# Performance work log

Measured on AMD Instinct MI355X. Metric: run time of the kernel, lower is better.

The kernel has to match this reference:

```python
import jax, jax.numpy as jnp
import numpy as np

NEG_INF = -1e30
EPS = 1e-7  # keras.backend.epsilon()


def _ctc_loss(y_true, y_pred):
    """Faithful CTC loss matching keras ctc_batch_cost + tf v1 ctc_loss.

    y_true: [B, L] int labels (no blanks), all rows full length L.
    y_pred: [B, T, C] probabilities; tf ctc_loss re-softmaxes log(p+eps).
    Blank index = C - 1. Returns loss [B, 1].
    """
    B, T, C = y_pred.shape
    L = y_true.shape[1]
    S = 2 * L + 1
    blank = C - 1

    # keras passes log(y_pred+eps) as logits; tf ctc_loss applies softmax
    lp = jax.nn.log_softmax(jnp.log(y_pred + EPS), axis=-1)  # [B,T,C]

    # extended label sequence: blank, l0, blank, l1, ..., blank  [B,S]
    ext = jnp.full((B, S), blank, dtype=y_true.dtype)
    ext = ext.at[:, 1::2].set(y_true)

    # skip transition (s-2 -> s) allowed iff ext[s] != blank and ext[s] != ext[s-2]
    same_as_2back = jnp.concatenate(
        [jnp.ones((B, 2), bool), ext[:, 2:] == ext[:, :-2]], axis=1)
    can_skip = (ext != blank) & (~same_as_2back)  # [B,S]

    # emission log-prob of each lattice state at each time: [B,T,S]
    lp_ext = jnp.take_along_axis(lp, ext[:, None, :], axis=2)

    # alpha init at t=0: only states 0 (blank) and 1 (first label) reachable
    alpha0 = jnp.full((B, S), NEG_INF, dtype=lp.dtype)
    alpha0 = alpha0.at[:, 0].set(lp_ext[:, 0, 0])
    alpha0 = alpha0.at[:, 1].set(lp_ext[:, 0, 1])

    pad1 = jnp.full((B, 1), NEG_INF, dtype=lp.dtype)
    pad2 = jnp.full((B, 2), NEG_INF, dtype=lp.dtype)

    def step(alpha, lp_t):
        a_stay = alpha
        a_prev = jnp.concatenate([pad1, alpha[:, :-1]], axis=1)
        a_skip = jnp.where(can_skip,
                           jnp.concatenate([pad2, alpha[:, :-2]], axis=1),
                           NEG_INF)
        m = jnp.maximum(a_stay, jnp.maximum(a_prev, a_skip))
        lse = m + jnp.log(jnp.exp(a_stay - m) + jnp.exp(a_prev - m)
                          + jnp.exp(a_skip - m))
        return lse + lp_t, None

    # scan over remaining T-1 time steps
    alphaT, _ = jax.lax.scan(step, alpha0, jnp.swapaxes(lp_ext, 0, 1)[1:])

    # total log-likelihood: end at last blank or last label
    loglik = jnp.logaddexp(alphaT[:, S - 1], alphaT[:, S - 2])
    return -loglik[:, None]  # [B,1], matches expand_dims(..., 1)


def setup_inputs() -> dict:
    key = jax.random.key(0)
    k1, k2 = jax.random.split(key)
    B, T, C, L = 128, 1024, 128, 128
    y_true = jax.random.randint(k1, (B, L), 0, C - 1, dtype=jnp.int32)
    y_pred = jax.random.uniform(k2, (B, T, C), dtype=jnp.float32)
    return {"y_true": y_true, "y_pred": y_pred}


def reference(y_true, y_pred):
    return _ctc_loss(y_true, y_pred)
```

## Files before the change

### kernel.cpp

```cpp
#include <hip/hip_runtime.h>

#define TT 1024
#define CC 128
#define LL 128
#define EPSF 1e-7f
#define LN2F 0.69314718055994531f

#define LOG2F(x) __builtin_amdgcn_logf(x)

typedef unsigned int uint;

template <int CTRL>
__device__ __forceinline__ int dpp_i(int old_, int x) {
  return __builtin_amdgcn_update_dpp(old_, x, CTRL, 0xf, 0xf, false);
}
__device__ __forceinline__ float dpp_shr1_f32(float x) {
  return __uint_as_float((uint)__builtin_amdgcn_update_dpp(
      0, (int)__float_as_uint(x), 0x138, 0xf, 0xf, true));
}

__device__ __forceinline__ uint bf16bits(float x) {
  uint u = __float_as_uint(x);
  return (u + 0x7fffu + ((u >> 16) & 1u)) >> 16;
}

#define GL16(gp, lp)                                            \
  __builtin_amdgcn_global_load_lds(                             \
      (const __attribute__((address_space(1))) void*)(gp),      \
      (__attribute__((address_space(3))) void*)(lp), 16, 0, 0)

__global__ __launch_bounds__(512) void prep_kernel(const int* __restrict__ yt,
                                                   const float* __restrict__ yp,
                                                   uint* __restrict__ ET,
                                                   float* __restrict__ EB) {
  const int tid = threadIdx.x;
  const int w = tid >> 6;
  const int L = tid & 63;
  const int b = blockIdx.x >> 7;
  const int tg = blockIdx.x & 127;
  const int t = tg * 8 + w;

  __shared__ float rowp[8][130];
  __shared__ uint tp[64][9];

  const float* P = yp + ((size_t)b * TT + t) * CC;
  const float2 v = *(const float2*)(P + 2 * L);
  float x = (v.x + EPSF) + (v.y + EPSF);
#pragma unroll
  for (int off = 32; off > 0; off >>= 1) x += __shfl_xor(x, off);
  const float r = 1.0f / x;
  const float er = EPSF * r;
  *(float2*)&rowp[w][2 * L] =
      make_float2(__builtin_fmaf(v.x, r, er), __builtin_fmaf(v.y, r, er));
  const int2 lab = *(const int2*)(yt + b * LL + 2 * L);
  if (L == 63) EB[b * TT + t] = __builtin_fmaf(v.y, r, er);
  __syncthreads();
  const float p1 = rowp[w][lab.x];
  const float p2 = rowp[w][lab.y];
  tp[L][w] = (bf16bits(p2) << 16) | bf16bits(p1);
  __syncthreads();
  if (tid < 128) {
    const int g4 = tid >> 6, Lo = tid & 63;
    uint4 val;
    val.x = tp[Lo][g4 * 4 + 0];
    val.y = tp[Lo][g4 * 4 + 1];
    val.z = tp[Lo][g4 * 4 + 2];
    val.w = tp[Lo][g4 * 4 + 3];
    ((uint4*)ET)[((size_t)(b * 256 + tg * 2 + g4) << 6) + Lo] = val;
  }
}


#define CTC_STEP(wv, pbf)                                   \
  do {                                                      \
    const float p1 = __uint_as_float((wv) << 16);           \
    const float p2 = __uint_as_float((wv) & 0xffff0000u);   \
    const float pb = (pbf);                                 \
    const float p3 = dpp_shr1_f32(a3);                      \
    const float n0 = (a0 + p3) * pb;                        \
    const float n1 = __builtin_fmaf(s1f, p3, a0 + a1) * p1; \
    const float n2 = (a2 + a1) * pb;                        \
    const float n3 = __builtin_fmaf(s3f, a1, a3 + a2) * p2; \
    const float n4 = (a4 + a3) * pb;                        \
    a0 = n0; a1 = n1; a2 = n2; a3 = n3; a4 = n4;            \
  } while (0)

#define CTC_QUAD(et, eb) \
  do {                   \
    CTC_STEP(et.x, eb.x); \
    CTC_STEP(et.y, eb.y); \
    CTC_STEP(et.z, eb.z); \
    CTC_STEP(et.w, eb.w); \
  } while (0)

#define CTC_RESCALE()                                                \
  do {                                                               \
    const float m = fmaxf(fmaxf(fmaxf(a0, a1), fmaxf(a2, a3)), a4);  \
    int ke = (int)(__float_as_uint(m) >> 23);                        \
    ke = max(ke, dpp_i<0x111>(ke, ke));                              \
    ke = max(ke, dpp_i<0x112>(ke, ke));                              \
    ke = max(ke, dpp_i<0x114>(ke, ke));                              \
    ke = max(ke, dpp_i<0x118>(ke, ke));                              \
    ke = max(ke, dpp_i<0x142>(ke, ke));                              \
    ke = max(ke, dpp_i<0x143>(ke, ke));                              \
    ke = __builtin_amdgcn_readlane(ke, 63);                          \
    int e = ke - 227;             \
    e = e < -127 ? -127 : e;                                         \
    const float sc = __uint_as_float((uint)(127 - e) << 23);         \
    a0 *= sc; a1 *= sc; a2 *= sc; a3 *= sc; a4 *= sc;                \
    ell += e;                                                        \
  } while (0)

__global__ __launch_bounds__(64) void scan_kernel(const int* __restrict__ yt,
                                                  const uint* __restrict__ ET,
                                                  const float* __restrict__ EB,
                                                  float* __restrict__ out) {
  const int b = blockIdx.x;
  const int L = threadIdx.x & 63;

  __shared__ uint4 ETl[4][8][64];
  __shared__ float4 EBl[256];

  const int2 lab = *(const int2*)(yt + b * LL + 2 * L);
  const int labm1 = __shfl_up(lab.y, 1);
  const float s1f = ((L > 0) && (lab.x != labm1)) ? 1.0f : 0.0f;
  const float s3f = (lab.y != lab.x) ? 1.0f : 0.0f;

  const uint4* Et = (const uint4*)ET + ((size_t)b << 14) + L;
  const float* Bp = EB + b * TT;

#pragma unroll
  for (int k = 0; k < 4; ++k)
    GL16(Bp + k * 256 + L * 4, (char*)EBl + k * 1024);
#pragma unroll
  for (int g = 0; g < 8; ++g) GL16(Et + g * 64, &ETl[0][g][0]);
#pragma unroll
  for (int g = 0; g < 8; ++g) GL16(Et + (8 + g) * 64, &ETl[1][g][0]);
  asm volatile("s_waitcnt vmcnt(8)" ::: "memory");

  uint4 etA = ETl[0][0][L], etB;
  float4 ebA = EBl[0], ebB;

  float a0 = (L == 0) ? 0x1.0p100f : 0.0f;
  float a1 = 0.0f, a2 = 0.0f, a3 = 0.0f, a4 = 0.0f;
  int ell = -100;

#pragma unroll 1
  for (int i = 0; i < 32; ++i) {
    {
      const int ip = (i + 2 < 32) ? (i + 2) : 31;
      const uint4* src = Et + (size_t)ip * 512;
      uint4* dst = &ETl[(i + 2) & 3][0][0];
#pragma unroll
      for (int g = 0; g < 8; ++g) GL16(src + g * 64, dst + g * 64);
    }
    const uint4* cur = &ETl[i & 3][0][0];
    const int ebi = i * 8;
    etB = cur[1 * 64 + L]; ebB = EBl[ebi + 1];
    CTC_QUAD(etA, ebA);
    etA = cur[2 * 64 + L]; ebA = EBl[ebi + 2];
    CTC_QUAD(etB, ebB);
    etB = cur[3 * 64 + L]; ebB = EBl[ebi + 3];
    CTC_QUAD(etA, ebA);
    etA = cur[4 * 64 + L]; ebA = EBl[ebi + 4];
    CTC_QUAD(etB, ebB);
    CTC_RESCALE();
    etB = cur[5 * 64 + L]; ebB = EBl[ebi + 5];
    CTC_QUAD(etA, ebA);
    etA = cur[6 * 64 + L]; ebA = EBl[ebi + 6];
    CTC_QUAD(etB, ebB);
    etB = cur[7 * 64 + L]; ebB = EBl[ebi + 7];
    CTC_QUAD(etA, ebA);
    asm volatile("s_waitcnt vmcnt(8)" ::: "memory");
    {
      const int ni = (i + 1 < 32) ? (i + 1) : 31;
      etA = ETl[(i + 1) & 3][0][L];
      ebA = EBl[ni * 8];
    }
    CTC_QUAD(etB, ebB);
    CTC_RESCALE();
  }

  if (L == 63) {
    float s = a3 + a4;
    if (s < 1e-37f) s = 1e-37f;
    out[b] = -LN2F * ((float)ell + LOG2F(s));
  }
}

extern "C" void kernel_launch(void* const* d_in, const int* in_sizes, int n_in,
                              void* d_out, int out_size, void* d_ws,
                              size_t ws_size, hipStream_t stream) {
  const int* yt = (const int*)d_in[0];
  const float* yp = (const float*)d_in[1];
  float* out = (float*)d_out;
  const int B = in_sizes[0] / LL;
  uint* ET = (uint*)d_ws;
  float* EB = (float*)((char*)d_ws + (size_t)B * 64 * TT * 4);
  hipLaunchKernelGGL(prep_kernel, dim3(B * 128), dim3(512), 0, stream, yt, yp,
                     ET, EB);
  hipLaunchKernelGGL(scan_kernel, dim3(B), dim3(64), 0, stream, yt, ET, EB,
                     out);
}
```

Measured before the change: 152.7 us.

## Split scan kernel into producer and consumer waves with block barriers

The scan kernel now runs two wavefronts per block. One wave issues the global-to-LDS prefetches of the emission tiles and the other runs the CTC recurrence, and the two synchronise with __syncthreads each iteration. The aim is to take the load-issue instructions and vmcnt waits off the serial compute wave's critical path. In exchange it adds a block barrier per 32-step chunk, and the compute wave now waits on the producer wave's progress.

```diff
diff --git a/kernel.cpp b/kernel.cpp
--- a/kernel.cpp
+++ b/kernel.cpp
@@ -9,6 +9,7 @@
 #define LOG2F(x) __builtin_amdgcn_logf(x)
 
 typedef unsigned int uint;
+typedef uint uintx4 __attribute__((ext_vector_type(4)));
 
 template <int CTRL>
 __device__ __forceinline__ int dpp_i(int old_, int x) {
@@ -28,6 +29,10 @@
   __builtin_amdgcn_global_load_lds(                             \
       (const __attribute__((address_space(1))) void*)(gp),      \
       (__attribute__((address_space(3))) void*)(lp), 16, 0, 0)
+#define GL4(gp, lp)                                             \
+  __builtin_amdgcn_global_load_lds(                             \
+      (const __attribute__((address_space(1))) void*)(gp),      \
+      (__attribute__((address_space(3))) void*)(lp), 4, 0, 0)
 
 __global__ __launch_bounds__(512) void prep_kernel(const int* __restrict__ yt,
                                                    const float* __restrict__ yp,
@@ -85,12 +90,12 @@
     a0 = n0; a1 = n1; a2 = n2; a3 = n3; a4 = n4;            \
   } while (0)
 
-#define CTC_QUAD(et, eb) \
-  do {                   \
-    CTC_STEP(et.x, eb.x); \
-    CTC_STEP(et.y, eb.y); \
-    CTC_STEP(et.z, eb.z); \
-    CTC_STEP(et.w, eb.w); \
+#define CTC_QUAD(et, eb)      \
+  do {                        \
+    CTC_STEP((et).x, (eb).x); \
+    CTC_STEP((et).y, (eb).y); \
+    CTC_STEP((et).z, (eb).z); \
+    CTC_STEP((et).w, (eb).w); \
   } while (0)
 
 #define CTC_RESCALE()                                                \
@@ -111,12 +116,14 @@
     ell += e;                                                        \
   } while (0)
 
-__global__ __launch_bounds__(64) void scan_kernel(const int* __restrict__ yt,
-                                                  const uint* __restrict__ ET,
-                                                  const float* __restrict__ EB,
-                                                  float* __restrict__ out) {
+__global__ __launch_bounds__(128) void scan_kernel(const int* __restrict__ yt,
+                                                   const uint* __restrict__ ET,
+                                                   const float* __restrict__ EB,
+                                                   float* __restrict__ out) {
   const int b = blockIdx.x;
-  const int L = threadIdx.x & 63;
+  const int tid = threadIdx.x;
+  const int L = tid & 63;
+  const int wv = tid >> 6;
 
   __shared__ uint4 ETl[4][8][64];
   __shared__ float4 EBl[256];
@@ -126,62 +133,65 @@
   const float s1f = ((L > 0) && (lab.x != labm1)) ? 1.0f : 0.0f;
   const float s3f = (lab.y != lab.x) ? 1.0f : 0.0f;
 
-  const uint4* Et = (const uint4*)ET + ((size_t)b << 14) + L;
+  const uintx4* Et = (const uintx4*)ET + ((size_t)b << 14) + L;
   const float* Bp = EB + b * TT;
 
-#pragma unroll
-  for (int k = 0; k < 4; ++k)
-    GL16(Bp + k * 256 + L * 4, (char*)EBl + k * 1024);
-#pragma unroll
-  for (int g = 0; g < 8; ++g) GL16(Et + g * 64, &ETl[0][g][0]);
-#pragma unroll
-  for (int g = 0; g < 8; ++g) GL16(Et + (8 + g) * 64, &ETl[1][g][0]);
-  asm volatile("s_waitcnt vmcnt(8)" ::: "memory");
-
-  uint4 etA = ETl[0][0][L], etB;
-  float4 ebA = EBl[0], ebB;
-
-  float a0 = (L == 0) ? 0x1.0p100f : 0.0f;
+  if (wv == 1) {
+#pragma unroll
+    for (int k = 0; k < 16; ++k) GL4(Bp + k * 64 + L, (char*)EBl + k * 256);
+#pragma unroll
+    for (int g = 0; g < 16; ++g) GL16(Et + g * 64, (char*)ETl + g * 1024);
+    asm volatile("s_waitcnt vmcnt(8)" ::: "memory");
+  }
+  __syncthreads();
+
+  uint4 etA, etB;
+  float4 ebA, ebB;
+  if (wv == 0) {
+    etA = ((const uint4*)ETl)[L];
+    ebA = EBl[0];
+  }
+
+  float a0 = (wv == 0 && L == 0) ? 0x1.0p100f : 0.0f;
   float a1 = 0.0f, a2 = 0.0f, a3 = 0.0f, a4 = 0.0f;
   int ell = -100;
 
 #pragma unroll 1
-  for (int i = 0; i < 32; ++i) {
-    {
-      const int ip = (i + 2 < 32) ? (i + 2) : 31;
-      const uint4* src = Et + (size_t)ip * 512;
-      uint4* dst = &ETl[(i + 2) & 3][0][0];
-#pragma unroll
-      for (int g = 0; g < 8; ++g) GL16(src + g * 64, dst + g * 64);
+  for (int kk = 0; kk < 32; ++kk) {
+    if (wv == 1) {
+      const int bb = (kk + 2 < 32) ? kk + 2 : 31;
+      const uintx4* src = Et + (size_t)bb * 512;
+      char* dst = (char*)ETl + (size_t)((kk + 2) & 3) * 8192;
+#pragma unroll
+      for (int g = 0; g < 8; ++g) GL16(src + g * 64, dst + g * 1024);
+      asm volatile("s_waitcnt vmcnt(8)" ::: "memory");
+    } else {
+      const uint4* cur = (const uint4*)ETl + (size_t)(kk & 3) * 512;
+      const int ebi = kk * 8;
+      etB = cur[1 * 64 + L]; ebB = EBl[ebi + 1];
+      CTC_QUAD(etA, ebA);
+      etA = cur[2 * 64 + L]; ebA = EBl[ebi + 2];
+      CTC_QUAD(etB, ebB);
+      etB = cur[3 * 64 + L]; ebB = EBl[ebi + 3];
+      CTC_QUAD(etA, ebA);
+      etA = cur[4 * 64 + L]; ebA = EBl[ebi + 4];
+      CTC_QUAD(etB, ebB);
+      CTC_RESCALE();
+      etB = cur[5 * 64 + L]; ebB = EBl[ebi + 5];
+      CTC_QUAD(etA, ebA);
+      etA = cur[6 * 64 + L]; ebA = EBl[ebi + 6];
+      CTC_QUAD(etB, ebB);
+      etB = cur[7 * 64 + L]; ebB = EBl[ebi + 7];
+      CTC_QUAD(etA, ebA);
+      etA = ((const uint4*)ETl)[(size_t)((kk + 1) & 3) * 512 + L];
+      ebA = EBl[(ebi + 8 < 256) ? ebi + 8 : 255];
+      CTC_QUAD(etB, ebB);
+      CTC_RESCALE();
     }
-    const uint4* cur = &ETl[i & 3][0][0];
-    const int ebi = i * 8;
-    etB = cur[1 * 64 + L]; ebB = EBl[ebi + 1];
-    CTC_QUAD(etA, ebA);
-    etA = cur[2 * 64 + L]; ebA = EBl[ebi + 2];
-    CTC_QUAD(etB, ebB);
-    etB = cur[3 * 64 + L]; ebB = EBl[ebi + 3];
-    CTC_QUAD(etA, ebA);
-    etA = cur[4 * 64 + L]; ebA = EBl[ebi + 4];
-    CTC_QUAD(etB, ebB);
-    CTC_RESCALE();
-    etB = cur[5 * 64 + L]; ebB = EBl[ebi + 5];
-    CTC_QUAD(etA, ebA);
-    etA = cur[6 * 64 + L]; ebA = EBl[ebi + 6];
-    CTC_QUAD(etB, ebB);
-    etB = cur[7 * 64 + L]; ebB = EBl[ebi + 7];
-    CTC_QUAD(etA, ebA);
-    asm volatile("s_waitcnt vmcnt(8)" ::: "memory");
-    {
-      const int ni = (i + 1 < 32) ? (i + 1) : 31;
-      etA = ETl[(i + 1) & 3][0][L];
-      ebA = EBl[ni * 8];
-    }
-    CTC_QUAD(etB, ebB);
-    CTC_RESCALE();
-  }
-
-  if (L == 63) {
+    __syncthreads();
+  }
+
+  if (tid == 63) {
     float s = a3 + a4;
     if (s < 1e-37f) s = 1e-37f;
     out[b] = -LN2F * ((float)ell + LOG2F(s));
@@ -199,6 +209,6 @@
   float* EB = (float*)((char*)d_ws + (size_t)B * 64 * TT * 4);
   hipLaunchKernelGGL(prep_kernel, dim3(B * 128), dim3(512), 0, stream, yt, yp,
                      ET, EB);
-  hipLaunchKernelGGL(scan_kernel, dim3(B), dim3(64), 0, stream, yt, ET, EB,
+  hipLaunchKernelGGL(scan_kernel, dim3(B), dim3(128), 0, stream, yt, ET, EB,
                      out);
 }
```

Measured after the change: 152.4 us. No clear change (-0.2%).
